# Kernel optimization log

Hardware: AMD Instinct MI355X
Metric: run time of the kernel (lower is better)

Reference implementation:

```python
import jax, jax.numpy as jnp
import numpy as np

EPS = 1e-5
N = 384
CZ = 128  # pair channels (c_z)
CH = 128  # hidden channels (c_hidden)


def _layer_norm(x, w, b):
    m = jnp.mean(x, axis=-1, keepdims=True)
    v = jnp.mean(jnp.square(x - m), axis=-1, keepdims=True)
    return (x - m) * jax.lax.rsqrt(v + EPS) * w + b


def setup_inputs() -> dict:
    key = jax.random.key(0)
    ks = jax.random.split(key, 8)
    s = 0.02  # weight init scale
    return {
        "z": jax.random.normal(ks[0], (1, N, N, CZ), jnp.float32),
        "ln_in_w": jnp.ones((2, CZ), jnp.float32),
        "ln_in_b": jnp.zeros((2, CZ), jnp.float32),
        "w_ag": jax.random.normal(ks[1], (2, CZ, CH), jnp.float32) * s,
        "b_ag": jnp.zeros((2, CH), jnp.float32),
        "w_ap": jax.random.normal(ks[2], (2, CZ, CH), jnp.float32) * s,
        "b_ap": jnp.zeros((2, CH), jnp.float32),
        "w_bg": jax.random.normal(ks[3], (2, CZ, CH), jnp.float32) * s,
        "b_bg": jnp.zeros((2, CH), jnp.float32),
        "w_bp": jax.random.normal(ks[4], (2, CZ, CH), jnp.float32) * s,
        "b_bp": jnp.zeros((2, CH), jnp.float32),
        "ln_out_w": jnp.ones((2, CH), jnp.float32),
        "ln_out_b": jnp.zeros((2, CH), jnp.float32),
        "w_z": jax.random.normal(ks[5], (2, CH, CZ), jnp.float32) * s,
        "b_z": jnp.zeros((2, CZ), jnp.float32),
        "w_g": jax.random.normal(ks[6], (2, CZ, CZ), jnp.float32) * s,
        "b_g": jnp.zeros((2, CZ), jnp.float32),
    }


def _tri_mul(z, outgoing, ln_in_w, ln_in_b, w_ag, b_ag, w_ap, b_ap,
             w_bg, b_bg, w_bp, b_bp, ln_out_w, ln_out_b, w_z, b_z, w_g, b_g):
    zn = _layer_norm(z, ln_in_w, ln_in_b)                      # [1,N,N,CZ]
    a = jax.nn.sigmoid(zn @ w_ag + b_ag) * (zn @ w_ap + b_ap)  # [1,N,N,CH]
    b = jax.nn.sigmoid(zn @ w_bg + b_bg) * (zn @ w_bp + b_bp)  # [1,N,N,CH]
    if outgoing:
        # p[i,k,c] = sum_j a[i,j,c] * b[k,j,c]
        p = jnp.einsum('bijc,bkjc->bikc', a, b)
    else:
        # p[i,k,c] = sum_j a[j,i,c] * b[j,k,c]
        p = jnp.einsum('bjic,bjkc->bikc', a, b)
    p = _layer_norm(p, ln_out_w, ln_out_b) @ w_z + b_z         # [1,N,N,CZ]
    g = jax.nn.sigmoid(zn @ w_g + b_g)
    return p * g


def reference(z, ln_in_w, ln_in_b, w_ag, b_ag, w_ap, b_ap, w_bg, b_bg,
              w_bp, b_bp, ln_out_w, ln_out_b, w_z, b_z, w_g, b_g):
    # idx 0: TriMulOut (outgoing=True), idx 1: TriMulIn (outgoing=False)
    for idx, outgoing in enumerate((True, False)):
        z = z + _tri_mul(z, outgoing,
                         ln_in_w[idx], ln_in_b[idx],
                         w_ag[idx], b_ag[idx], w_ap[idx], b_ap[idx],
                         w_bg[idx], b_bg[idx], w_bp[idx], b_bp[idx],
                         ln_out_w[idx], ln_out_b[idx],
                         w_z[idx], b_z[idx], w_g[idx], b_g[idx])
    return z
```

## Files before the change

### kernel.cpp

```cpp
#include <hip/hip_runtime.h>


constexpr int NS = 384;
constexpr int NN = NS * NS;

using bf16x8 = __attribute__((ext_vector_type(8))) __bf16;
using f32x4  = __attribute__((ext_vector_type(4))) float;

__device__ inline void load16_to_lds(const __bf16* g, __bf16* lds) {
  auto* gp = reinterpret_cast<const __attribute__((address_space(1))) unsigned int*>(
      reinterpret_cast<uintptr_t>(g));
  auto* lp = reinterpret_cast<__attribute__((address_space(3))) unsigned int*>(
      reinterpret_cast<uintptr_t>(lds));
  __builtin_amdgcn_global_load_lds(gp, lp, 16, 0, 0);
}

__global__ __launch_bounds__(256) void prep_weights(
    const float* __restrict__ w_ag, const float* __restrict__ w_ap,
    const float* __restrict__ w_bg, const float* __restrict__ w_bp,
    const float* __restrict__ w_g,  const float* __restrict__ w_z,
    __bf16* __restrict__ wsw)
{
  int gid  = blockIdx.x * 256 + threadIdx.x;
  int mat  = gid >> 11;
  int slot = gid & 2047;
  int lane = slot & 63;
  int tb   = (slot >> 6) & 7;
  int s    = slot >> 9;
  int pass = mat / 6, which = mat % 6;
  const float* W;
  switch (which) {
    case 0: W = w_ag; break; case 1: W = w_ap; break; case 2: W = w_bg; break;
    case 3: W = w_bp; break; case 4: W = w_g;  break; default: W = w_z;
  }
  W += pass * 16384;
  int n0 = tb * 16 + (lane & 15);
  int k0 = s * 32 + (lane >> 4) * 8;
  __bf16* dst = wsw + ((size_t)mat * 2048 + slot) * 8;
#pragma unroll
  for (int j = 0; j < 8; ++j) dst[j] = (__bf16)W[(k0 + j) * 128 + n0];
}

__global__ __launch_bounds__(256) void proj_kernel(
    const float* __restrict__ zsrc, const float* __restrict__ lnw, const float* __restrict__ lnb,
    const __bf16* __restrict__ wsw5,
    const float* __restrict__ bag, const float* __restrict__ bap,
    const float* __restrict__ bbg, const float* __restrict__ bbp, const float* __restrict__ bgg,
    __bf16* __restrict__ a_t, __bf16* __restrict__ b_t, __bf16* __restrict__ g_out, int mode)
{
  __shared__ __bf16 zn[64][136];
  int tid = threadIdx.x;
  int rb = 0, r2 = 0;
  size_t pstart = 0;
  if (mode == 0) pstart = (size_t)blockIdx.x * 64;
  else { rb = blockIdx.x / NS; r2 = blockIdx.x % NS; }

  {
    int row = tid >> 2, q = tid & 3;
    size_t zoff = (mode == 0) ? (pstart + row) * 128
                              : ((size_t)(64 * rb + row) * NS + r2) * 128;
    const float4* zp = (const float4*)(zsrc + zoff) + q * 8;
    float4 v[8];
#pragma unroll
    for (int u = 0; u < 8; ++u) v[u] = zp[u];
    float s1 = 0.f, s2 = 0.f;
#pragma unroll
    for (int u = 0; u < 8; ++u) {
      float4 t = v[u];
      s1 += t.x + t.y + t.z + t.w;
      s2 += t.x * t.x + t.y * t.y + t.z * t.z + t.w * t.w;
    }
    s1 += __shfl_xor(s1, 1); s2 += __shfl_xor(s2, 1);
    s1 += __shfl_xor(s1, 2); s2 += __shfl_xor(s2, 2);
    float mean = s1 * (1.0f / 128.0f);
    float var  = s2 * (1.0f / 128.0f) - mean * mean;
    float rstd = rsqrtf(var + 1e-5f);
#pragma unroll
    for (int u = 0; u < 8; ++u) {
      int c0 = q * 32 + u * 4;
      float4 t  = v[u];
      float4 w4 = *(const float4*)(lnw + c0);
      float4 b4 = *(const float4*)(lnb + c0);
      zn[row][c0 + 0] = (__bf16)((t.x - mean) * rstd * w4.x + b4.x);
      zn[row][c0 + 1] = (__bf16)((t.y - mean) * rstd * w4.y + b4.y);
      zn[row][c0 + 2] = (__bf16)((t.z - mean) * rstd * w4.z + b4.z);
      zn[row][c0 + 3] = (__bf16)((t.w - mean) * rstd * w4.w + b4.w);
    }
  }
  __syncthreads();

  const int wv = tid >> 6;
  const int lane = tid & 63;
  const int lm = lane & 15;
  const int lq = lane >> 4;
  const size_t wposbase = (mode == 0) ? pstart : ((size_t)r2 * NS + 64 * rb);

  bf16x8 znf[4][4];
#pragma unroll
  for (int nt = 0; nt < 4; ++nt)
#pragma unroll
    for (int s = 0; s < 4; ++s)
      znf[nt][s] = *(const bf16x8*)(&zn[16 * nt + lm][32 * s + 8 * lq]);

#pragma unroll
  for (int grp = 0; grp < 3; ++grp) {
    const __bf16* wA;
    const __bf16* wB = nullptr;
    const float* pbA;
    const float* pbB = nullptr;
    __bf16* dst = nullptr;
    if (grp == 0)      { wA = wsw5;             wB = wsw5 + 16384;   pbA = bag; pbB = bap; dst = a_t; }
    else if (grp == 1) { wA = wsw5 + 2 * 16384; wB = wsw5 + 3 * 16384; pbA = bbg; pbB = bbp; dst = b_t; }
    else               { wA = wsw5 + 4 * 16384; pbA = bgg; }

#pragma unroll
    for (int mbi = 0; mbi < 2; ++mbi) {
      const int mb = 2 * wv + mbi;
      bf16x8 fA[4], fB[4];
#pragma unroll
      for (int s = 0; s < 4; ++s) {
        fA[s] = *(const bf16x8*)(wA + ((size_t)((s * 8 + mb) * 64 + lane)) * 8);
        if (grp < 2) fB[s] = *(const bf16x8*)(wB + ((size_t)((s * 8 + mb) * 64 + lane)) * 8);
      }
      if (grp < 2) {
        float biasA[4], biasB[4];
#pragma unroll
        for (int r = 0; r < 4; ++r) {
          int cc = 16 * mb + 4 * lq + r;
          biasA[r] = pbA[cc];
          biasB[r] = pbB[cc];
        }
#pragma unroll
        for (int nt = 0; nt < 4; ++nt) {
          f32x4 acc0 = {0.f, 0.f, 0.f, 0.f}, acc1 = {0.f, 0.f, 0.f, 0.f};
#pragma unroll
          for (int s = 0; s < 4; ++s) {
            acc0 = __builtin_amdgcn_mfma_f32_16x16x32_bf16(fA[s], znf[nt][s], acc0, 0, 0, 0);
            acc1 = __builtin_amdgcn_mfma_f32_16x16x32_bf16(fB[s], znf[nt][s], acc1, 0, 0, 0);
          }
          size_t wp = wposbase + 16 * nt + lm;
#pragma unroll
          for (int r = 0; r < 4; ++r) {
            int cc = 16 * mb + 4 * lq + r;
            float xg = acc0[r] + biasA[r];
            float xp = acc1[r] + biasB[r];
            float val = xp / (1.0f + __expf(-xg));
            dst[(size_t)cc * NN + wp] = (__bf16)val;
          }
        }
      } else {
        float biasG = pbA[16 * mb + lm];
#pragma unroll
        for (int nt = 0; nt < 4; ++nt) {
          f32x4 acc = {0.f, 0.f, 0.f, 0.f};
#pragma unroll
          for (int s = 0; s < 4; ++s)
            acc = __builtin_amdgcn_mfma_f32_16x16x32_bf16(znf[nt][s], fA[s], acc, 0, 0, 0);
          int cc = 16 * mb + lm;
#pragma unroll
          for (int r = 0; r < 4; ++r) {
            int pos = 16 * nt + 4 * lq + r;
            size_t gp = (mode == 0) ? (pstart + pos) * 128
                                    : ((size_t)(64 * rb + pos) * NS + r2) * 128;
            float val = 1.0f / (1.0f + __expf(-(acc[r] + biasG)));
            g_out[gp + cc] = (__bf16)val;
          }
        }
      }
    }
  }
}

__global__ __launch_bounds__(256) void tri_kernel(
    const __bf16* __restrict__ a_t, const __bf16* __restrict__ b_t, __bf16* __restrict__ p_t)
{
  __shared__ __bf16 As[128 * 64];
  __shared__ __bf16 Bs[128 * 64];
  int c  = blockIdx.z;
  int i0 = blockIdx.x * 128, k0 = blockIdx.y * 128;
  const __bf16* Ab = a_t + (size_t)c * NN;
  const __bf16* Bb = b_t + (size_t)c * NN;
  int tid = threadIdx.x, wv = tid >> 6, lane = tid & 63;
  int lm = lane & 15, lq = lane >> 4;
  int lrow = lane >> 3;
  int lsl  = lane & 7;
  int lch  = lsl ^ lrow;
  f32x4 acc[4][4];
#pragma unroll
  for (int mi = 0; mi < 4; ++mi)
#pragma unroll
    for (int ni = 0; ni < 4; ++ni) acc[mi][ni] = {0.f, 0.f, 0.f, 0.f};
  const int rowA_half = 64 * (wv & 1), colB_half = 64 * (wv >> 1);

  for (int kk = 0; kk < 384; kk += 64) {
    __syncthreads();
#pragma unroll
    for (int v = 0; v < 4; ++v) {
      int rgrp = 4 * wv + v;
      int r = 8 * rgrp + lrow;
      load16_to_lds(Ab + (size_t)(i0 + r) * NS + kk + lch * 8, As + rgrp * 512);
      load16_to_lds(Bb + (size_t)(k0 + r) * NS + kk + lch * 8, Bs + rgrp * 512);
    }
    __syncthreads();
#pragma unroll
    for (int s = 0; s < 2; ++s) {
      bf16x8 bfr[4], afr[4];
#pragma unroll
      for (int ni = 0; ni < 4; ++ni)
        bfr[ni] = *(const bf16x8*)(Bs + (colB_half + 16 * ni + lm) * 64 +
                                   ((4 * s + lq) ^ (lm & 7)) * 8);
#pragma unroll
      for (int mi = 0; mi < 4; ++mi)
        afr[mi] = *(const bf16x8*)(As + (rowA_half + 16 * mi + lm) * 64 +
                                   ((4 * s + lq) ^ (lm & 7)) * 8);
#pragma unroll
      for (int mi = 0; mi < 4; ++mi)
#pragma unroll
        for (int ni = 0; ni < 4; ++ni)
          acc[mi][ni] = __builtin_amdgcn_mfma_f32_16x16x32_bf16(afr[mi], bfr[ni], acc[mi][ni], 0, 0, 0);
    }
  }
#pragma unroll
  for (int mi = 0; mi < 4; ++mi)
#pragma unroll
    for (int ni = 0; ni < 4; ++ni)
#pragma unroll
      for (int r = 0; r < 4; ++r) {
        int row = i0 + rowA_half + 16 * mi + 4 * lq + r;
        int col = k0 + colB_half + 16 * ni + lm;
        p_t[(size_t)c * NN + (size_t)row * NS + col] = (__bf16)acc[mi][ni][r];
      }
}

__global__ __launch_bounds__(256) void out_kernel(
    const __bf16* __restrict__ p_t, const __bf16* __restrict__ g_in,
    const float* __restrict__ z_in, float* __restrict__ z_out,
    const float* __restrict__ lnw, const float* __restrict__ lnb,
    const __bf16* __restrict__ wz, const float* __restrict__ bz)
{
  __shared__ __bf16 pl[64][136];
  int tid = threadIdx.x;
  size_t base = (size_t)blockIdx.x * 64;

  {
    int c2 = tid >> 1, hf = tid & 1;
    const __bf16* src = p_t + (size_t)c2 * NN + base + hf * 32;
    bf16x8 v0 = ((const bf16x8*)src)[0];
    bf16x8 v1 = ((const bf16x8*)src)[1];
    bf16x8 v2 = ((const bf16x8*)src)[2];
    bf16x8 v3 = ((const bf16x8*)src)[3];
#pragma unroll
    for (int j = 0; j < 8; ++j) pl[hf * 32 + j][c2] = v0[j];
#pragma unroll
    for (int j = 0; j < 8; ++j) pl[hf * 32 + 8 + j][c2] = v1[j];
#pragma unroll
    for (int j = 0; j < 8; ++j) pl[hf * 32 + 16 + j][c2] = v2[j];
#pragma unroll
    for (int j = 0; j < 8; ++j) pl[hf * 32 + 24 + j][c2] = v3[j];
  }
  __syncthreads();

  {
    int row = tid >> 2, q = tid & 3;
    bf16x8 pv[4];
#pragma unroll
    for (int s = 0; s < 4; ++s) pv[s] = *(const bf16x8*)(&pl[row][q * 32 + 8 * s]);
    float s1 = 0.f, s2 = 0.f;
#pragma unroll
    for (int s = 0; s < 4; ++s)
#pragma unroll
      for (int j = 0; j < 8; ++j) { float f = (float)pv[s][j]; s1 += f; s2 += f * f; }
    s1 += __shfl_xor(s1, 1); s2 += __shfl_xor(s2, 1);
    s1 += __shfl_xor(s1, 2); s2 += __shfl_xor(s2, 2);
    float mean = s1 * (1.0f / 128.0f);
    float var  = s2 * (1.0f / 128.0f) - mean * mean;
    float rstd = rsqrtf(var + 1e-5f);
#pragma unroll
    for (int s = 0; s < 4; ++s) {
#pragma unroll
      for (int j = 0; j < 8; ++j) {
        int cc = q * 32 + 8 * s + j;
        float f = ((float)pv[s][j] - mean) * rstd * lnw[cc] + lnb[cc];
        pv[s][j] = (__bf16)f;
      }
      *(bf16x8*)(&pl[row][q * 32 + 8 * s]) = pv[s];
    }
  }
  __syncthreads();

  int wv = tid >> 6, lane = tid & 63, lm = lane & 15, lq = lane >> 4;
  bf16x8 wzf[2][4];
  float bzv[2];
#pragma unroll
  for (int nbi = 0; nbi < 2; ++nbi) {
    int nb = 2 * wv + nbi;
    bzv[nbi] = bz[16 * nb + lm];
#pragma unroll
    for (int s = 0; s < 4; ++s)
      wzf[nbi][s] = *(const bf16x8*)(wz + ((size_t)((s * 8 + nb) * 64 + lane)) * 8);
  }
#pragma unroll
  for (int mt = 0; mt < 4; ++mt) {
    bf16x8 af[4];
#pragma unroll
    for (int s = 0; s < 4; ++s)
      af[s] = *(const bf16x8*)(&pl[16 * mt + lm][32 * s + 8 * lq]);
#pragma unroll
    for (int nbi = 0; nbi < 2; ++nbi) {
      f32x4 acc = {0.f, 0.f, 0.f, 0.f};
#pragma unroll
      for (int s = 0; s < 4; ++s)
        acc = __builtin_amdgcn_mfma_f32_16x16x32_bf16(af[s], wzf[nbi][s], acc, 0, 0, 0);
      int cz = 16 * (2 * wv + nbi) + lm;
#pragma unroll
      for (int r = 0; r < 4; ++r) {
        int pos = 16 * mt + 4 * lq + r;
        size_t idx = (base + pos) * 128 + cz;
        float gv  = (float)g_in[idx];
        float res = (acc[r] + bzv[nbi]) * gv + z_in[idx];
        z_out[idx] = res;
      }
    }
  }
}

extern "C" void kernel_launch(void* const* d_in, const int* in_sizes, int n_in,
                              void* d_out, int out_size, void* d_ws, size_t ws_size,
                              hipStream_t stream) {
  (void)in_sizes; (void)n_in; (void)out_size; (void)ws_size;
  const float* z        = (const float*)d_in[0];
  const float* ln_in_w  = (const float*)d_in[1];
  const float* ln_in_b  = (const float*)d_in[2];
  const float* w_ag     = (const float*)d_in[3];
  const float* b_ag     = (const float*)d_in[4];
  const float* w_ap     = (const float*)d_in[5];
  const float* b_ap     = (const float*)d_in[6];
  const float* w_bg     = (const float*)d_in[7];
  const float* b_bg     = (const float*)d_in[8];
  const float* w_bp     = (const float*)d_in[9];
  const float* b_bp     = (const float*)d_in[10];
  const float* ln_out_w = (const float*)d_in[11];
  const float* ln_out_b = (const float*)d_in[12];
  const float* w_z      = (const float*)d_in[13];
  const float* b_z      = (const float*)d_in[14];
  const float* w_g      = (const float*)d_in[15];
  const float* b_g      = (const float*)d_in[16];
  float* out = (float*)d_out;

  __bf16* wsw = (__bf16*)d_ws;
  __bf16* a_t = wsw + 12 * 16384;
  __bf16* b_t = a_t + (size_t)NN * 128;
  __bf16* g_b = b_t + (size_t)NN * 128;
  __bf16* p_t = g_b + (size_t)NN * 128;

  prep_weights<<<96, 256, 0, stream>>>(w_ag, w_ap, w_bg, w_bp, w_g, w_z, wsw);

  for (int idx = 0; idx < 2; ++idx) {
    const float* zsrc = (idx == 0) ? z : out;
    const __bf16* wsw5 = wsw + (size_t)idx * 6 * 16384;
    proj_kernel<<<2304, 256, 0, stream>>>(
        zsrc, ln_in_w + idx * 128, ln_in_b + idx * 128, wsw5,
        b_ag + idx * 128, b_ap + idx * 128, b_bg + idx * 128, b_bp + idx * 128,
        b_g + idx * 128, a_t, b_t, g_b, idx);
    tri_kernel<<<dim3(3, 3, 128), 256, 0, stream>>>(a_t, b_t, p_t);
    out_kernel<<<2304, 256, 0, stream>>>(
        p_t, g_b, zsrc, out, ln_out_w + idx * 128, ln_out_b + idx * 128,
        wsw5 + 5 * 16384, b_z + idx * 128);
  }
}
```

Before: 462.7 us.

## Recompute output gate in out_kernel and vectorize proj_kernel stores

The gate projection and sigmoid move from proj_kernel into out_kernel, which recomputes the input layer norm from z and runs an extra MFMA GEMM with w_g. This removes the bf16 gate buffer's global write and read. proj_kernel also swaps MFMA operand order so each lane writes four consecutive positions as one packed 8-byte store instead of scattered 2-byte stores. In exchange out_kernel does extra layer-norm work, uses another LDS tile and holds more weight registers, which may lower occupancy.

```diff
diff --git a/kernel.cpp b/kernel.cpp
--- a/kernel.cpp
+++ b/kernel.cpp
@@ -5,6 +5,7 @@
 constexpr int NN = NS * NS;
 
 using bf16x8 = __attribute__((ext_vector_type(8))) __bf16;
+using bf16x4 = __attribute__((ext_vector_type(4))) __bf16;
 using f32x4  = __attribute__((ext_vector_type(4))) float;
 
 __device__ inline void load16_to_lds(const __bf16* g, __bf16* lds) {
@@ -45,8 +46,8 @@
     const float* __restrict__ zsrc, const float* __restrict__ lnw, const float* __restrict__ lnb,
     const __bf16* __restrict__ wsw5,
     const float* __restrict__ bag, const float* __restrict__ bap,
-    const float* __restrict__ bbg, const float* __restrict__ bbp, const float* __restrict__ bgg,
-    __bf16* __restrict__ a_t, __bf16* __restrict__ b_t, __bf16* __restrict__ g_out, int mode)
+    const float* __restrict__ bbg, const float* __restrict__ bbp,
+    __bf16* __restrict__ a_t, __bf16* __restrict__ b_t, int mode)
 {
   __shared__ __bf16 zn[64][136];
   int tid = threadIdx.x;
@@ -103,69 +104,42 @@
       znf[nt][s] = *(const bf16x8*)(&zn[16 * nt + lm][32 * s + 8 * lq]);
 
 #pragma unroll
-  for (int grp = 0; grp < 3; ++grp) {
-    const __bf16* wA;
-    const __bf16* wB = nullptr;
-    const float* pbA;
-    const float* pbB = nullptr;
-    __bf16* dst = nullptr;
-    if (grp == 0)      { wA = wsw5;             wB = wsw5 + 16384;   pbA = bag; pbB = bap; dst = a_t; }
-    else if (grp == 1) { wA = wsw5 + 2 * 16384; wB = wsw5 + 3 * 16384; pbA = bbg; pbB = bbp; dst = b_t; }
-    else               { wA = wsw5 + 4 * 16384; pbA = bgg; }
+  for (int grp = 0; grp < 2; ++grp) {
+    const __bf16* wG = wsw5 + (size_t)(2 * grp) * 16384;
+    const __bf16* wP = wG + 16384;
+    const float* pg = grp ? bbg : bag;
+    const float* pp = grp ? bbp : bap;
+    __bf16* dst = grp ? b_t : a_t;
 
 #pragma unroll
     for (int mbi = 0; mbi < 2; ++mbi) {
       const int mb = 2 * wv + mbi;
-      bf16x8 fA[4], fB[4];
+      bf16x8 fG[4], fP[4];
 #pragma unroll
       for (int s = 0; s < 4; ++s) {
-        fA[s] = *(const bf16x8*)(wA + ((size_t)((s * 8 + mb) * 64 + lane)) * 8);
-        if (grp < 2) fB[s] = *(const bf16x8*)(wB + ((size_t)((s * 8 + mb) * 64 + lane)) * 8);
-      }
-      if (grp < 2) {
-        float biasA[4], biasB[4];
+        fG[s] = *(const bf16x8*)(wG + ((size_t)((s * 8 + mb) * 64 + lane)) * 8);
+        fP[s] = *(const bf16x8*)(wP + ((size_t)((s * 8 + mb) * 64 + lane)) * 8);
+      }
+      const int cc = 16 * mb + lm;
+      float bG = pg[cc];
+      float bP = pp[cc];
+      __bf16* drow = dst + (size_t)cc * NN + wposbase + 4 * lq;
+#pragma unroll
+      for (int nt = 0; nt < 4; ++nt) {
+        f32x4 acc0 = {0.f, 0.f, 0.f, 0.f}, acc1 = {0.f, 0.f, 0.f, 0.f};
+#pragma unroll
+        for (int s = 0; s < 4; ++s) {
+          acc0 = __builtin_amdgcn_mfma_f32_16x16x32_bf16(znf[nt][s], fG[s], acc0, 0, 0, 0);
+          acc1 = __builtin_amdgcn_mfma_f32_16x16x32_bf16(znf[nt][s], fP[s], acc1, 0, 0, 0);
+        }
+        bf16x4 pk;
 #pragma unroll
         for (int r = 0; r < 4; ++r) {
-          int cc = 16 * mb + 4 * lq + r;
-          biasA[r] = pbA[cc];
-          biasB[r] = pbB[cc];
+          float xg = acc0[r] + bG;
+          float xp = acc1[r] + bP;
+          pk[r] = (__bf16)(xp / (1.0f + __expf(-xg)));
         }
-#pragma unroll
-        for (int nt = 0; nt < 4; ++nt) {
-          f32x4 acc0 = {0.f, 0.f, 0.f, 0.f}, acc1 = {0.f, 0.f, 0.f, 0.f};
-#pragma unroll
-          for (int s = 0; s < 4; ++s) {
-            acc0 = __builtin_amdgcn_mfma_f32_16x16x32_bf16(fA[s], znf[nt][s], acc0, 0, 0, 0);
-            acc1 = __builtin_amdgcn_mfma_f32_16x16x32_bf16(fB[s], znf[nt][s], acc1, 0, 0, 0);
-          }
-          size_t wp = wposbase + 16 * nt + lm;
-#pragma unroll
-          for (int r = 0; r < 4; ++r) {
-            int cc = 16 * mb + 4 * lq + r;
-            float xg = acc0[r] + biasA[r];
-            float xp = acc1[r] + biasB[r];
-            float val = xp / (1.0f + __expf(-xg));
-            dst[(size_t)cc * NN + wp] = (__bf16)val;
-          }
-        }
-      } else {
-        float biasG = pbA[16 * mb + lm];
-#pragma unroll
-        for (int nt = 0; nt < 4; ++nt) {
-          f32x4 acc = {0.f, 0.f, 0.f, 0.f};
-#pragma unroll
-          for (int s = 0; s < 4; ++s)
-            acc = __builtin_amdgcn_mfma_f32_16x16x32_bf16(znf[nt][s], fA[s], acc, 0, 0, 0);
-          int cc = 16 * mb + lm;
-#pragma unroll
-          for (int r = 0; r < 4; ++r) {
-            int pos = 16 * nt + 4 * lq + r;
-            size_t gp = (mode == 0) ? (pstart + pos) * 128
-                                    : ((size_t)(64 * rb + pos) * NS + r2) * 128;
-            float val = 1.0f / (1.0f + __expf(-(acc[r] + biasG)));
-            g_out[gp + cc] = (__bf16)val;
-          }
-        }
+        *(bf16x4*)(drow + 16 * nt) = pk;
       }
     }
   }
@@ -233,14 +207,48 @@
 }
 
 __global__ __launch_bounds__(256) void out_kernel(
-    const __bf16* __restrict__ p_t, const __bf16* __restrict__ g_in,
+    const __bf16* __restrict__ p_t,
     const float* __restrict__ z_in, float* __restrict__ z_out,
-    const float* __restrict__ lnw, const float* __restrict__ lnb,
-    const __bf16* __restrict__ wz, const float* __restrict__ bz)
+    const float* __restrict__ lniw, const float* __restrict__ lnib,
+    const float* __restrict__ lnow, const float* __restrict__ lnob,
+    const __bf16* __restrict__ wz, const float* __restrict__ bz,
+    const __bf16* __restrict__ wg, const float* __restrict__ bg)
 {
   __shared__ __bf16 pl[64][136];
+  __shared__ __bf16 znl[64][136];
   int tid = threadIdx.x;
   size_t base = (size_t)blockIdx.x * 64;
+
+  {
+    int row = tid >> 2, q = tid & 3;
+    const float4* zp = (const float4*)(z_in + (base + row) * 128) + q * 8;
+    float4 v[8];
+#pragma unroll
+    for (int u = 0; u < 8; ++u) v[u] = zp[u];
+    float s1 = 0.f, s2 = 0.f;
+#pragma unroll
+    for (int u = 0; u < 8; ++u) {
+      float4 t = v[u];
+      s1 += t.x + t.y + t.z + t.w;
+      s2 += t.x * t.x + t.y * t.y + t.z * t.z + t.w * t.w;
+    }
+    s1 += __shfl_xor(s1, 1); s2 += __shfl_xor(s2, 1);
+    s1 += __shfl_xor(s1, 2); s2 += __shfl_xor(s2, 2);
+    float mean = s1 * (1.0f / 128.0f);
+    float var  = s2 * (1.0f / 128.0f) - mean * mean;
+    float rstd = rsqrtf(var + 1e-5f);
+#pragma unroll
+    for (int u = 0; u < 8; ++u) {
+      int c0 = q * 32 + u * 4;
+      float4 t  = v[u];
+      float4 w4 = *(const float4*)(lniw + c0);
+      float4 b4 = *(const float4*)(lnib + c0);
+      znl[row][c0 + 0] = (__bf16)((t.x - mean) * rstd * w4.x + b4.x);
+      znl[row][c0 + 1] = (__bf16)((t.y - mean) * rstd * w4.y + b4.y);
+      znl[row][c0 + 2] = (__bf16)((t.z - mean) * rstd * w4.z + b4.z);
+      znl[row][c0 + 3] = (__bf16)((t.w - mean) * rstd * w4.w + b4.w);
+    }
+  }
 
   {
     int c2 = tid >> 1, hf = tid & 1;
@@ -280,7 +288,7 @@
 #pragma unroll
       for (int j = 0; j < 8; ++j) {
         int cc = q * 32 + 8 * s + j;
-        float f = ((float)pv[s][j] - mean) * rstd * lnw[cc] + lnb[cc];
+        float f = ((float)pv[s][j] - mean) * rstd * lnow[cc] + lnob[cc];
         pv[s][j] = (__bf16)f;
       }
       *(bf16x8*)(&pl[row][q * 32 + 8 * s]) = pv[s];
@@ -289,35 +297,43 @@
   __syncthreads();
 
   int wv = tid >> 6, lane = tid & 63, lm = lane & 15, lq = lane >> 4;
-  bf16x8 wzf[2][4];
-  float bzv[2];
+  bf16x8 wzf[2][4], wgf[2][4];
+  float bzv[2], bgv[2];
 #pragma unroll
   for (int nbi = 0; nbi < 2; ++nbi) {
     int nb = 2 * wv + nbi;
     bzv[nbi] = bz[16 * nb + lm];
-#pragma unroll
-    for (int s = 0; s < 4; ++s)
+    bgv[nbi] = bg[16 * nb + lm];
+#pragma unroll
+    for (int s = 0; s < 4; ++s) {
       wzf[nbi][s] = *(const bf16x8*)(wz + ((size_t)((s * 8 + nb) * 64 + lane)) * 8);
+      wgf[nbi][s] = *(const bf16x8*)(wg + ((size_t)((s * 8 + nb) * 64 + lane)) * 8);
+    }
   }
 #pragma unroll
   for (int mt = 0; mt < 4; ++mt) {
-    bf16x8 af[4];
-#pragma unroll
-    for (int s = 0; s < 4; ++s)
+    bf16x8 af[4], zf[4];
+#pragma unroll
+    for (int s = 0; s < 4; ++s) {
       af[s] = *(const bf16x8*)(&pl[16 * mt + lm][32 * s + 8 * lq]);
+      zf[s] = *(const bf16x8*)(&znl[16 * mt + lm][32 * s + 8 * lq]);
+    }
 #pragma unroll
     for (int nbi = 0; nbi < 2; ++nbi) {
-      f32x4 acc = {0.f, 0.f, 0.f, 0.f};
-#pragma unroll
-      for (int s = 0; s < 4; ++s)
-        acc = __builtin_amdgcn_mfma_f32_16x16x32_bf16(af[s], wzf[nbi][s], acc, 0, 0, 0);
+      f32x4 accp = {0.f, 0.f, 0.f, 0.f};
+      f32x4 accg = {0.f, 0.f, 0.f, 0.f};
+#pragma unroll
+      for (int s = 0; s < 4; ++s) {
+        accp = __builtin_amdgcn_mfma_f32_16x16x32_bf16(af[s], wzf[nbi][s], accp, 0, 0, 0);
+        accg = __builtin_amdgcn_mfma_f32_16x16x32_bf16(zf[s], wgf[nbi][s], accg, 0, 0, 0);
+      }
       int cz = 16 * (2 * wv + nbi) + lm;
 #pragma unroll
       for (int r = 0; r < 4; ++r) {
         int pos = 16 * mt + 4 * lq + r;
         size_t idx = (base + pos) * 128 + cz;
-        float gv  = (float)g_in[idx];
-        float res = (acc[r] + bzv[nbi]) * gv + z_in[idx];
+        float gv  = 1.0f / (1.0f + __expf(-(accg[r] + bgv[nbi])));
+        float res = (accp[r] + bzv[nbi]) * gv + z_in[idx];
         z_out[idx] = res;
       }
     }
@@ -350,8 +366,7 @@
   __bf16* wsw = (__bf16*)d_ws;
   __bf16* a_t = wsw + 12 * 16384;
   __bf16* b_t = a_t + (size_t)NN * 128;
-  __bf16* g_b = b_t + (size_t)NN * 128;
-  __bf16* p_t = g_b + (size_t)NN * 128;
+  __bf16* p_t = b_t + (size_t)NN * 128;
 
   prep_weights<<<96, 256, 0, stream>>>(w_ag, w_ap, w_bg, w_bp, w_g, w_z, wsw);
 
@@ -361,10 +376,13 @@
     proj_kernel<<<2304, 256, 0, stream>>>(
         zsrc, ln_in_w + idx * 128, ln_in_b + idx * 128, wsw5,
         b_ag + idx * 128, b_ap + idx * 128, b_bg + idx * 128, b_bp + idx * 128,
-        b_g + idx * 128, a_t, b_t, g_b, idx);
+        a_t, b_t, idx);
     tri_kernel<<<dim3(3, 3, 128), 256, 0, stream>>>(a_t, b_t, p_t);
     out_kernel<<<2304, 256, 0, stream>>>(
-        p_t, g_b, zsrc, out, ln_out_w + idx * 128, ln_out_b + idx * 128,
-        wsw5 + 5 * 16384, b_z + idx * 128);
-  }
-}
+        p_t, zsrc, out,
+        ln_in_w + idx * 128, ln_in_b + idx * 128,
+        ln_out_w + idx * 128, ln_out_b + idx * 128,
+        wsw5 + 5 * 16384, b_z + idx * 128,
+        wsw5 + 4 * 16384, b_g + idx * 128);
+  }
+}
```

Result: faster. 451.2 us (-2.5%).
